# Kernel tuning notes

Measured on AMD Instinct MI355X. Metric: run time of the kernel, lower is better.

## Reference

```python
import jax, jax.numpy as jnp
import numpy as np

B, X_DIM, U_DIM, PHI, HID = 1024, 32, 8, 128, 128


def _mlp(x, W1, b1, W2, b2, W3, b3, W4, b4):
    # backbone: Linear-Tanh x3 then Linear, per get_encoder (env != 'kitchen')
    h = jnp.tanh(x @ W1 + b1)
    h = jnp.tanh(h @ W2 + b2)
    h = jnp.tanh(h @ W3 + b3)
    return h @ W4 + b4


def setup_inputs() -> dict:
    key = jax.random.key(0)
    ks = jax.random.split(key, 12)
    x = jax.random.normal(ks[0], (B, X_DIM), jnp.float32)
    # posterior params per log_predictive_prob docstring (batch-leading)
    Q = jax.random.normal(ks[1], (B, U_DIM, 1, PHI), jnp.float32) * (4.0 / (np.sqrt(PHI) + np.sqrt(U_DIM)))
    # PSD-like L, mimicking L_asym @ L_asym^T + diag(exp(L_base))
    A = jax.random.normal(ks[2], (B, U_DIM, PHI, PHI), jnp.float32) / PHI
    Lbase = jnp.exp(jnp.linspace(-5.0, 0.0, PHI, dtype=jnp.float32))
    L = jnp.einsum('bupq,burq->bupr', A, A) + jnp.diag(Lbase)[None, None]
    s = lambda fan: 1.0 / np.sqrt(fan)
    W1 = jax.random.normal(ks[3], (X_DIM, HID), jnp.float32) * s(X_DIM)
    b1 = jnp.zeros((HID,), jnp.float32)
    W2 = jax.random.normal(ks[4], (HID, HID), jnp.float32) * s(HID)
    b2 = jnp.zeros((HID,), jnp.float32)
    W3 = jax.random.normal(ks[5], (HID, HID), jnp.float32) * s(HID)
    b3 = jnp.zeros((HID,), jnp.float32)
    W4 = jax.random.normal(ks[6], (HID, PHI), jnp.float32) * s(HID)
    b4 = jnp.zeros((PHI,), jnp.float32)
    logSigEps = jnp.log(jnp.full((U_DIM,), 0.1, jnp.float32))
    return {"x": x, "Q": Q, "L": L, "W1": W1, "b1": b1, "W2": W2, "b2": b2,
            "W3": W3, "b3": b3, "W4": W4, "b4": b4, "logSigEps": logSigEps}


def reference(x, Q, L, W1, b1, W2, b2, W3, b3, W4, b4, logSigEps):
    # encoder: phi vector (B, PHI); torch reshapes to (B, 1, PHI, 1) purely for matmul broadcasting
    phiv = _mlp(x, W1, b1, W2, b2, W3, b3, W4, b4)          # (B, P)
    Lphi = jnp.einsum('bupq,bq->bup', L, phiv)               # L @ phi -> (B, U, P)
    sigfactor = 1.0 + jnp.einsum('bp,bup->bu', phiv, Lphi)   # 1 + phi^T L phi -> (B, U)
    # mu = (K @ phi).squeeze(-1), K = Q @ L  ->  Q @ (L @ phi)
    mu = jnp.einsum('bup,bup->bu', Q[:, :, 0, :], Lphi)[..., None]  # (B, U, 1)
    SigEps = jnp.diag(jnp.exp(logSigEps))                    # (U, U)
    sig = SigEps[None] * sigfactor[:, :, None]               # (B, U, U)
    return mu, sig
```

## Files before the change

### kernel.cpp

```cpp
#include <hip/hip_runtime.h>
#include <hip/hip_bf16.h>
#include <math.h>

#define BATCH 1024
#define X_DIM 32
#define U_DIM 8
#define PHI 128
#define HID 128

#define NLINE 320

typedef float f4 __attribute__((ext_vector_type(4)));

__device__ __forceinline__ float fast_tanh(float x) {
    return 1.0f - 2.0f / (__expf(2.0f * x) + 1.0f);
}

__global__ __launch_bounds__(512) void fused_kernel(
    const float* __restrict__ x,
    const float* __restrict__ Q,
    const float* __restrict__ L,
    const float* __restrict__ W1, const float* __restrict__ b1,
    const float* __restrict__ W2, const float* __restrict__ b2,
    const float* __restrict__ W3, const float* __restrict__ b3,
    const float* __restrict__ W4, const float* __restrict__ b4,
    const float* __restrict__ logSigEps,
    float* __restrict__ mu_out,
    float* __restrict__ sig_out)
{
    const int b = blockIdx.x;
    const int t = threadIdx.x;

    __shared__ float sx[X_DIM];
    __shared__ float h[HID];
    __shared__ alignas(16) float s_phi[PHI];
    __shared__ alignas(16) float s_Q[U_DIM * PHI];
    __shared__ unsigned short s_tabL[NLINE];
    __shared__ unsigned short s_tabU[NLINE];

    {
        const float2* Qg = (const float2*)(Q + (size_t)b * (U_DIM * PHI));
        ((float2*)s_Q)[t] = Qg[t];
    }
    if (t < X_DIM) sx[t] = x[b * X_DIM + t];

    if (t < 256) {
        const int r = t & 127;
        const int m = r >> 5;
        const int s = 16 * m * (m - 1) + (r & 31) * m;
        if (t < 128) {
            const int base = r + s;
            for (int lc = 0; lc <= m; ++lc)
                s_tabL[base + lc] = (unsigned short)((r << 9) | (lc << 7));
        } else {
            const int base = 4 * r - s;
            for (int lc = m; lc < 4; ++lc)
                s_tabU[base + (lc - m)] = (unsigned short)((r << 9) | (lc << 7));
        }
    }
    __syncthreads();

    float acc;
    if (t < HID) {
        acc = b1[t];
#pragma unroll
        for (int k = 0; k < X_DIM; ++k) acc += sx[k] * W1[k * HID + t];
        h[t] = fast_tanh(acc);
    }
    __syncthreads();
    if (t < HID) {
        acc = b2[t];
#pragma unroll 8
        for (int k = 0; k < HID; ++k) acc += h[k] * W2[k * HID + t];
        acc = fast_tanh(acc);
    }
    __syncthreads();
    if (t < HID) h[t] = acc;
    __syncthreads();
    if (t < HID) {
        acc = b3[t];
#pragma unroll 8
        for (int k = 0; k < HID; ++k) acc += h[k] * W3[k * HID + t];
        acc = fast_tanh(acc);
    }
    __syncthreads();
    if (t < HID) h[t] = acc;
    __syncthreads();
    if (t < HID) {
        acc = b4[t];
#pragma unroll 8
        for (int k = 0; k < HID; ++k) acc += h[k] * W4[k * HID + t];
        s_phi[t] = acc;
    }
    __syncthreads();

    const int u  = t >> 6;
    const int l  = t & 63;
    const int g  = l >> 3;
    const int tl = l & 7;
    const bool isUp = (u & 1) != 0;
    const int  dk   = isUp ? -1 : 1;

    const unsigned short* __restrict__ tab = isUp ? s_tabU : s_tabL;

    const char* __restrict__ Lbase =
        (const char*)(L + ((size_t)(b * U_DIM + u)) * (PHI * PHI));
    const float* __restrict__ Qu = s_Q + u * PHI;
    const f4* __restrict__ s_phi4 = (const f4*)s_phi;
    const f4* __restrict__ Qu4 = (const f4*)Qu;

    const int tl16 = tl << 4;

    int offs[4];
#pragma unroll
    for (int k = 0; k < 4; ++k) offs[k] = (int)tab[(k << 3) + g] + tl16;

    float accm = 0.0f, accf = 0.0f;
#pragma unroll
    for (int i = 0; i < 40; ++i) {
        const int off = offs[i & 3];
        if (i + 4 < 40) offs[i & 3] = (int)tab[((i + 4) << 3) + g] + tl16;

        const f4 v = __builtin_nontemporal_load((const f4*)(Lbase + off));
        const int r = off >> 9;
        const int c = (off >> 4) & 31;
        const float phir = s_phi[r];
        const float Qr   = Qu[r];
        const f4 ph = s_phi4[c];
        const f4 Qv = Qu4[c];
        int ek = isUp ? (r - 4 * c) : (4 * c - r);

        {
            const float w = (ek < 0) ? 1.0f : ((ek == 0) ? 0.5f : 0.0f);
            const float tv = w * v.x;
            accm += tv * (Qr * ph.x + Qv.x * phir);
            accf += tv * (phir * ph.x);
        }
        ek += dk;
        {
            const float w = (ek < 0) ? 1.0f : ((ek == 0) ? 0.5f : 0.0f);
            const float tv = w * v.y;
            accm += tv * (Qr * ph.y + Qv.y * phir);
            accf += tv * (phir * ph.y);
        }
        ek += dk;
        {
            const float w = (ek < 0) ? 1.0f : ((ek == 0) ? 0.5f : 0.0f);
            const float tv = w * v.z;
            accm += tv * (Qr * ph.z + Qv.z * phir);
            accf += tv * (phir * ph.z);
        }
        ek += dk;
        {
            const float w = (ek < 0) ? 1.0f : ((ek == 0) ? 0.5f : 0.0f);
            const float tv = w * v.w;
            accm += tv * (Qr * ph.w + Qv.w * phir);
            accf += tv * (phir * ph.w);
        }
    }

#pragma unroll
    for (int off = 1; off < 64; off <<= 1) {
        accm += __shfl_xor(accm, off);
        accf += __shfl_xor(accf, off);
    }

    const int bu = b * U_DIM + u;
    if (l == 0) mu_out[bu] = accm;
    if (l < U_DIM) {
        const float sf = 1.0f + 2.0f * accf;
        sig_out[(size_t)bu * U_DIM + l] = (l == u) ? __expf(logSigEps[u]) * sf : 0.0f;
    }
}

extern "C" void kernel_launch(void* const* d_in, const int* in_sizes, int n_in,
                              void* d_out, int out_size, void* d_ws, size_t ws_size,
                              hipStream_t stream)
{
    const float* x         = (const float*)d_in[0];
    const float* Q         = (const float*)d_in[1];
    const float* L         = (const float*)d_in[2];
    const float* W1        = (const float*)d_in[3];
    const float* b1        = (const float*)d_in[4];
    const float* W2        = (const float*)d_in[5];
    const float* b2        = (const float*)d_in[6];
    const float* W3        = (const float*)d_in[7];
    const float* b3        = (const float*)d_in[8];
    const float* W4        = (const float*)d_in[9];
    const float* b4        = (const float*)d_in[10];
    const float* logSigEps = (const float*)d_in[11];

    float* out     = (float*)d_out;
    float* mu_out  = out;
    float* sig_out = out + BATCH * U_DIM;

    fused_kernel<<<BATCH, 512, 0, stream>>>(x, Q, L,
                                            W1, b1, W2, b2, W3, b3, W4, b4,
                                            logSigEps, mu_out, sig_out);
}
```

Before: 70.46 us.

## Split each batch row across two 256-thread blocks covering four u each

Each batch element now gets two blocks of 256 threads, each handling half of the U dimension, instead of one 512-thread block. This gives more, smaller blocks so the GPU can schedule them more flexibly and the L streaming phase can overlap across blocks. The cost is that the small MLP is computed twice per batch element, which adds redundant weight reads and serial latency.

Result: no change. 70.49 us (+0.0%).

```diff
diff --git a/kernel.cpp b/kernel.cpp
--- a/kernel.cpp
+++ b/kernel.cpp
@@ -16,7 +16,7 @@
     return 1.0f - 2.0f / (__expf(2.0f * x) + 1.0f);
 }
 
-__global__ __launch_bounds__(512) void fused_kernel(
+__global__ __launch_bounds__(256) void fused_kernel(
     const float* __restrict__ x,
     const float* __restrict__ Q,
     const float* __restrict__ L,
@@ -28,23 +28,25 @@
     float* __restrict__ mu_out,
     float* __restrict__ sig_out)
 {
-    const int b = blockIdx.x;
-    const int t = threadIdx.x;
+    const int b    = blockIdx.x >> 1;
+    const int half = blockIdx.x & 1;
+    const int t    = threadIdx.x;
 
     __shared__ float sx[X_DIM];
     __shared__ float h[HID];
     __shared__ alignas(16) float s_phi[PHI];
-    __shared__ alignas(16) float s_Q[U_DIM * PHI];
+    __shared__ alignas(16) float s_Q[4 * PHI];
     __shared__ unsigned short s_tabL[NLINE];
     __shared__ unsigned short s_tabU[NLINE];
 
     {
-        const float2* Qg = (const float2*)(Q + (size_t)b * (U_DIM * PHI));
+        const float2* Qg = (const float2*)(Q + (size_t)b * (U_DIM * PHI)
+                                             + (size_t)half * (4 * PHI));
         ((float2*)s_Q)[t] = Qg[t];
     }
     if (t < X_DIM) sx[t] = x[b * X_DIM + t];
 
-    if (t < 256) {
+    {
         const int r = t & 127;
         const int m = r >> 5;
         const int s = 16 * m * (m - 1) + (r & 31) * m;
@@ -94,7 +96,8 @@
     }
     __syncthreads();
 
-    const int u  = t >> 6;
+    const int w  = t >> 6;
+    const int u  = (half << 2) | w;
     const int l  = t & 63;
     const int g  = l >> 3;
     const int tl = l & 7;
@@ -105,7 +108,7 @@
 
     const char* __restrict__ Lbase =
         (const char*)(L + ((size_t)(b * U_DIM + u)) * (PHI * PHI));
-    const float* __restrict__ Qu = s_Q + u * PHI;
+    const float* __restrict__ Qu = s_Q + w * PHI;
     const f4* __restrict__ s_phi4 = (const f4*)s_phi;
     const f4* __restrict__ Qu4 = (const f4*)Qu;
 
@@ -131,29 +134,29 @@
         int ek = isUp ? (r - 4 * c) : (4 * c - r);
 
         {
-            const float w = (ek < 0) ? 1.0f : ((ek == 0) ? 0.5f : 0.0f);
-            const float tv = w * v.x;
+            const float w0 = (ek < 0) ? 1.0f : ((ek == 0) ? 0.5f : 0.0f);
+            const float tv = w0 * v.x;
             accm += tv * (Qr * ph.x + Qv.x * phir);
             accf += tv * (phir * ph.x);
         }
         ek += dk;
         {
-            const float w = (ek < 0) ? 1.0f : ((ek == 0) ? 0.5f : 0.0f);
-            const float tv = w * v.y;
+            const float w0 = (ek < 0) ? 1.0f : ((ek == 0) ? 0.5f : 0.0f);
+            const float tv = w0 * v.y;
             accm += tv * (Qr * ph.y + Qv.y * phir);
             accf += tv * (phir * ph.y);
         }
         ek += dk;
         {
-            const float w = (ek < 0) ? 1.0f : ((ek == 0) ? 0.5f : 0.0f);
-            const float tv = w * v.z;
+            const float w0 = (ek < 0) ? 1.0f : ((ek == 0) ? 0.5f : 0.0f);
+            const float tv = w0 * v.z;
             accm += tv * (Qr * ph.z + Qv.z * phir);
             accf += tv * (phir * ph.z);
         }
         ek += dk;
         {
-            const float w = (ek < 0) ? 1.0f : ((ek == 0) ? 0.5f : 0.0f);
-            const float tv = w * v.w;
+            const float w0 = (ek < 0) ? 1.0f : ((ek == 0) ? 0.5f : 0.0f);
+            const float tv = w0 * v.w;
             accm += tv * (Qr * ph.w + Qv.w * phir);
             accf += tv * (phir * ph.w);
         }
@@ -194,7 +197,7 @@
     float* mu_out  = out;
     float* sig_out = out + BATCH * U_DIM;
 
-    fused_kernel<<<BATCH, 512, 0, stream>>>(x, Q, L,
-                                            W1, b1, W2, b2, W3, b3, W4, b4,
-                                            logSigEps, mu_out, sig_out);
+    fused_kernel<<<2 * BATCH, 256, 0, stream>>>(x, Q, L,
+                                                W1, b1, W2, b2, W3, b3, W4, b4,
+                                                logSigEps, mu_out, sig_out);
 }
```
